# Kernel tuning notes

Measured on AMD Instinct MI355X. Metric: run time of the kernel, lower is better.

## Reference

```python
import jax, jax.numpy as jnp
import numpy as np

H, W = 16, 16
DIM = 512
HEADS = 8
DIM_HEAD = 64
INNER = HEADS * DIM_HEAD  # 512
B = 8
N = H * W  # 256
SCALE = DIM_HEAD ** -0.5
EPS = 1e-5


def _index_map(h, w):
    # index_map[n, m] = dx * (2w-1) + dy with dx = x-i+h-1, dy = y-j+w-1
    xs = np.arange(h)
    ys = np.arange(w)
    dx = xs[:, None] - xs[None, :] + h - 1            # (h, h)
    dy = ys[:, None] - ys[None, :] + w - 1            # (w, w)
    idx = dx[:, None, :, None] * (2 * w - 1) + dy[None, :, None, :]  # (h, w, h, w)
    return idx.reshape(h * w, h * w).astype(np.int32)


def setup_inputs() -> dict:
    key = jax.random.key(0)
    ks = jax.random.split(key, 5)
    x = jax.random.normal(ks[0], (B, N, DIM), dtype=jnp.float32)
    ln_g = jnp.ones((DIM,), jnp.float32)
    ln_b = jnp.zeros((DIM,), jnp.float32)
    w_qkv = jax.random.normal(ks[1], (DIM, 3 * INNER), jnp.float32) * 0.02
    unique_params = jax.random.normal(ks[2], ((2 * H - 1) * (2 * W - 1), INNER), jnp.float32) * 0.02
    w_out = jax.random.normal(ks[3], (INNER, DIM), jnp.float32) * 0.02
    b_out = jnp.zeros((DIM,), jnp.float32)
    idx_map = jnp.asarray(_index_map(H, W))  # (N, N) int32
    return {"x": x, "ln_g": ln_g, "ln_b": ln_b, "w_qkv": w_qkv,
            "unique_params": unique_params, "w_out": w_out, "b_out": b_out,
            "idx_map": idx_map}


def reference(x, ln_g, ln_b, w_qkv, unique_params, w_out, b_out, idx_map):
    b, n, _ = x.shape
    # LayerNorm
    mu = jnp.mean(x, axis=-1, keepdims=True)
    var = jnp.mean(jnp.square(x - mu), axis=-1, keepdims=True)
    xn = (x - mu) * jax.lax.rsqrt(var + EPS) * ln_g + ln_b
    # qkv projection (no bias)
    qkv = xn @ w_qkv                                  # (b, n, 3*inner)
    q, k, v = jnp.split(qkv, 3, axis=-1)
    q = q.reshape(b, n, HEADS, DIM_HEAD)
    k = k.reshape(b, n, HEADS, DIM_HEAD)
    v = v.reshape(b, n, HEADS, DIM_HEAD)
    # attention scores
    dots = jnp.einsum('bnhd,bmhd->bhnm', q, k) * SCALE
    attn = jax.nn.softmax(dots, axis=-1)              # (b, h, n, m)
    # relative-position table: (n, m, h, d)
    rpos = unique_params[idx_map].reshape(n, n, HEADS, DIM_HEAD)
    # out[b,h,n,d] = sum_m attn[b,h,n,m] * (v[b,m,h,d] + rpos[n,m,h,d])
    out = jnp.einsum('bhnm,bmhd->bnhd', attn, v) \
        + jnp.einsum('bhnm,nmhd->bnhd', attn, rpos)
    out = out.reshape(b, n, INNER)
    return out @ w_out + b_out
```

## Files before the change

### kernel.cpp

```cpp
#include <hip/hip_runtime.h>
#include <math.h>

#define NB 8
#define SEQ 256
#define DIMC 512
#define NHEAD 8
#define DHEAD 64
#define SCALEF 0.125f

typedef __attribute__((ext_vector_type(8))) short s16x8;
typedef __attribute__((ext_vector_type(4))) float f32x4;

typedef __attribute__((address_space(3))) unsigned int lds_u32_t;
typedef const __attribute__((address_space(1))) unsigned int g_u32_t;
static __device__ __forceinline__ void gl_lds16(const void* gsrc, void* ldst) {
  __builtin_amdgcn_global_load_lds((g_u32_t*)gsrc, (lds_u32_t*)ldst, 16, 0, 0);
}

static __device__ __forceinline__ unsigned short f2bf(float f) {
  union { float f; unsigned u; } c; c.f = f;
  unsigned r = c.u + 0x7FFF + ((c.u >> 16) & 1);
  return (unsigned short)(r >> 16);
}

static __device__ void tcast_body(const float* __restrict__ W,
    unsigned short* __restrict__ WT, int K, int N, int n0, int k0, int t,
    float (*tile)[65]) {
#pragma unroll
  for (int i = 0; i < 16; ++i) {
    const int idx = i * 256 + t;
    const int kl = idx >> 6, nl = idx & 63;
    tile[kl][nl] = W[(size_t)(k0 + kl) * N + n0 + nl];
  }
  __syncthreads();
#pragma unroll
  for (int i = 0; i < 16; ++i) {
    const int idx = i * 256 + t;
    const int nl = idx >> 6, kl = idx & 63;
    WT[(size_t)(n0 + nl) * K + k0 + kl] = f2bf(tile[kl][nl]);
  }
}

__global__ __launch_bounds__(256) void prep_kernel(const float* __restrict__ x,
    const float* __restrict__ g, const float* __restrict__ bta,
    const float* __restrict__ w_qkv, const float* __restrict__ w_out,
    const float* __restrict__ up, unsigned short* __restrict__ xnb,
    unsigned short* __restrict__ wqt, unsigned short* __restrict__ wot,
    unsigned short* __restrict__ upT) {
  __shared__ float tile[64][65];
  __shared__ float sh_s[4], sh_q[4];
  const int t = threadIdx.x;
  const int bid = blockIdx.x;
  if (bid < 192) {
    tcast_body(w_qkv, wqt, 512, 1536, (bid % 24) * 64, (bid / 24) * 64, t, tile);
  } else if (bid < 256) {
    const int b2 = bid - 192;
    tcast_body(w_out, wot, 512, 512, (b2 % 8) * 64, (b2 / 8) * 64, t, tile);
  } else if (bid < 384) {
    const int b2 = bid - 256;
    const int k0 = (b2 >> 3) * 64, n0 = (b2 & 7) * 64;
#pragma unroll
    for (int i = 0; i < 16; ++i) {
      const int idx = i * 256 + t;
      const int kl = idx >> 6, nl = idx & 63;
      const int k = k0 + kl;
      tile[kl][nl] = (k < 961) ? up[(size_t)k * 512 + n0 + nl] : 0.0f;
    }
    __syncthreads();
#pragma unroll
    for (int i = 0; i < 16; ++i) {
      const int idx = i * 256 + t;
      const int nl = idx >> 6, kl = idx & 63;
      if (k0 + kl < 992)
        upT[(size_t)(n0 + nl) * 992 + k0 + kl] = f2bf(tile[kl][nl]);
    }
  } else {
    const int row = bid - 384;
    const float2 v = ((const float2*)(x + (size_t)row * DIMC))[t];
    float s = v.x + v.y;
    float q = v.x * v.x + v.y * v.y;
#pragma unroll
    for (int off = 32; off > 0; off >>= 1) {
      s += __shfl_down(s, off);
      q += __shfl_down(q, off);
    }
    const int wave = t >> 6, lane = t & 63;
    if (lane == 0) { sh_s[wave] = s; sh_q[wave] = q; }
    __syncthreads();
    const float fs = sh_s[0] + sh_s[1] + sh_s[2] + sh_s[3];
    const float fq = sh_q[0] + sh_q[1] + sh_q[2] + sh_q[3];
    const float mean = fs * (1.0f / DIMC);
    const float inv = rsqrtf(fq * (1.0f / DIMC) - mean * mean + 1e-5f);
    const float2 gv = ((const float2*)g)[t];
    const float2 bv = ((const float2*)bta)[t];
    ushort2 o;
    o.x = f2bf((v.x - mean) * inv * gv.x + bv.x);
    o.y = f2bf((v.y - mean) * inv * gv.y + bv.y);
    ((ushort2*)(xnb + (size_t)row * DIMC))[t] = o;
  }
}

template <int BM, int BN, bool BIAS, bool OUTBF, bool VSPLIT>
__global__ __launch_bounds__(256) void mfma_gemm_bt(
    const unsigned short* __restrict__ A, const unsigned short* __restrict__ BT,
    const float* __restrict__ bias, void* __restrict__ Cv,
    unsigned short* __restrict__ vtb, int M, int K, int N) {
  constexpr int TR = BM / 32;
  constexpr int TC = BN / 32;
  __shared__ unsigned short As[BM * 32];
  __shared__ unsigned short Bs[BN * 32];
  const int t = threadIdx.x;
  const int wave = t >> 6, lane = t & 63;
  const int wr = wave >> 1, wc = wave & 1;
  const int bm = blockIdx.x * BM, bn = blockIdx.y * BN;

  f32x4 acc[TR][TC] = {};

  const int fr = lane & 15, q4 = lane >> 4;
  const int kBlocks = K >> 5;
  for (int kb = 0; kb < kBlocks; ++kb) {
    const int k0 = kb << 5;
    __syncthreads();
#pragma unroll
    for (int c = 0; c < (BM * 4 + 255) / 256; ++c) {
      const int p = c * 256 + t;
      if (BM * 4 % 256 == 0 || p < BM * 4) {
        const int row = p >> 2;
        const int jl = (p & 3) ^ ((row >> 1) & 3);
        gl_lds16(A + (size_t)(bm + row) * K + k0 + jl * 8,
                 As + (size_t)(c * 256 + wave * 64) * 8);
      }
    }
#pragma unroll
    for (int c = 0; c < (BN * 4 + 255) / 256; ++c) {
      const int p = c * 256 + t;
      if (BN * 4 % 256 == 0 || p < BN * 4) {
        const int row = p >> 2;
        const int jl = (p & 3) ^ ((row >> 1) & 3);
        gl_lds16(BT + (size_t)(bn + row) * K + k0 + jl * 8,
                 Bs + (size_t)(c * 256 + wave * 64) * 8);
      }
    }
    __syncthreads();
    s16x8 af[TR], bfr[TC];
#pragma unroll
    for (int i = 0; i < TR; ++i) {
      const int row = wr * (BM / 2) + i * 16 + fr;
      const int jp = q4 ^ ((row >> 1) & 3);
      af[i] = *(const s16x8*)(As + row * 32 + jp * 8);
    }
#pragma unroll
    for (int j = 0; j < TC; ++j) {
      const int row = wc * (BN / 2) + j * 16 + fr;
      const int jp = q4 ^ ((row >> 1) & 3);
      bfr[j] = *(const s16x8*)(Bs + row * 32 + jp * 8);
    }
#pragma unroll
    for (int i = 0; i < TR; ++i)
#pragma unroll
      for (int j = 0; j < TC; ++j)
        acc[i][j] = __builtin_amdgcn_mfma_f32_16x16x32_bf16(af[i], bfr[j],
                                                            acc[i][j], 0, 0, 0);
  }
  if (VSPLIT && bn >= 1024) {
#pragma unroll
    for (int i = 0; i < TR; ++i) {
#pragma unroll
      for (int j = 0; j < TC; ++j) {
        const int hc = bn - 1024 + wc * (BN / 2) + j * 16 + fr;
        const int h = hc >> 6, d = hc & 63;
#pragma unroll
        for (int r = 0; r < 4; ++r) {
          const int row = bm + wr * (BM / 2) + i * 16 + q4 * 4 + r;
          const int b = row >> 8, m = row & 255;
          vtb[(size_t)((b * 8 + h) * 64 + d) * 256 + m] = f2bf(acc[i][j][r]);
        }
      }
    }
    return;
  }
#pragma unroll
  for (int i = 0; i < TR; ++i) {
#pragma unroll
    for (int j = 0; j < TC; ++j) {
      const int col = bn + wc * (BN / 2) + j * 16 + fr;
      const float bv = BIAS ? bias[col] : 0.0f;
#pragma unroll
      for (int r = 0; r < 4; ++r) {
        const int row = bm + wr * (BM / 2) + i * 16 + q4 * 4 + r;
        if constexpr (OUTBF) {
          ((unsigned short*)Cv)[(size_t)row * N + col] = f2bf(acc[i][j][r] + bv);
        } else {
          ((float*)Cv)[(size_t)row * N + col] = acc[i][j][r] + bv;
        }
      }
    }
  }
}

#define PSTR 264
#define ASTR 552
__global__ __launch_bounds__(128) void attn_rpos_kernel(
    const unsigned short* __restrict__ qkvb,
    const unsigned short* __restrict__ vtb,
    const unsigned short* __restrict__ upT,
    unsigned short* __restrict__ ob) {
  __shared__ unsigned short ascat[32 * ASTR];
  __shared__ unsigned short p_lds[32 * PSTR];
  const int bh = blockIdx.y, b = bh >> 3, h = bh & 7;
  const int n0 = blockIdx.x * 32;
  const int t = threadIdx.x, wave = t >> 6, lane = t & 63;
  const int fr = lane & 15, q4 = lane >> 4;
  const int kwin0 = ((n0 >> 4) * 31) & ~7;

  {
    const s16x8 z = {0, 0, 0, 0, 0, 0, 0, 0};
#pragma unroll
    for (int i = 0; i < 18; ++i) {
      const int idx = i * 128 + t;
      if (idx < 32 * ASTR / 8) *(s16x8*)(ascat + idx * 8) = z;
    }
  }

  s16x8 qf[2];
  {
    const size_t qrow = (size_t)(b * SEQ + n0 + wave * 16 + fr) * 1536 + h * 64;
#pragma unroll
    for (int ks = 0; ks < 2; ++ks)
      qf[ks] = *(const s16x8*)(qkvb + qrow + ks * 32 + q4 * 8);
  }

  f32x4 s[16];
#pragma unroll
  for (int mt = 0; mt < 16; ++mt) s[mt] = (f32x4){0.f, 0.f, 0.f, 0.f};
  {
    const unsigned short* kb = qkvb + (size_t)(b * SEQ + fr) * 1536 + 512 + h * 64;
#pragma unroll
    for (int ks = 0; ks < 2; ++ks)
#pragma unroll
      for (int mt = 0; mt < 16; ++mt) {
        const s16x8 kf =
            *(const s16x8*)(kb + (size_t)mt * (16 * 1536) + ks * 32 + q4 * 8);
        s[mt] = __builtin_amdgcn_mfma_f32_16x16x32_bf16(qf[ks], kf, s[mt], 0, 0, 0);
      }
  }

  float mx[4] = {-1e30f, -1e30f, -1e30f, -1e30f};
#pragma unroll
  for (int mt = 0; mt < 16; ++mt)
#pragma unroll
    for (int r = 0; r < 4; ++r) {
      s[mt][r] *= SCALEF;
      mx[r] = fmaxf(mx[r], s[mt][r]);
    }
#pragma unroll
  for (int r = 0; r < 4; ++r) {
    mx[r] = fmaxf(mx[r], __shfl_xor(mx[r], 1));
    mx[r] = fmaxf(mx[r], __shfl_xor(mx[r], 2));
    mx[r] = fmaxf(mx[r], __shfl_xor(mx[r], 4));
    mx[r] = fmaxf(mx[r], __shfl_xor(mx[r], 8));
  }
  float sum[4] = {0.f, 0.f, 0.f, 0.f};
#pragma unroll
  for (int mt = 0; mt < 16; ++mt)
#pragma unroll
    for (int r = 0; r < 4; ++r) {
      s[mt][r] = __expf(s[mt][r] - mx[r]);
      sum[r] += s[mt][r];
    }
#pragma unroll
  for (int r = 0; r < 4; ++r) {
    sum[r] += __shfl_xor(sum[r], 1);
    sum[r] += __shfl_xor(sum[r], 2);
    sum[r] += __shfl_xor(sum[r], 4);
    sum[r] += __shfl_xor(sum[r], 8);
  }
  const float invs[4] = {1.0f / sum[0], 1.0f / sum[1], 1.0f / sum[2],
                         1.0f / sum[3]};

  __syncthreads();

  const int nb = wave * 16 + q4 * 4;
#pragma unroll
  for (int r = 0; r < 4; ++r) {
    const int n = n0 + nb + r;
    const int xn = n >> 4, yn = n & 15;
    const int cb = (xn + 15) * 31 + (yn - fr + 15) - kwin0;
    unsigned short* arow = ascat + (nb + r) * ASTR + cb;
    unsigned short* prow = p_lds + (nb + r) * PSTR + fr;
#pragma unroll
    for (int mt = 0; mt < 16; ++mt) {
      const unsigned short pb = f2bf(s[mt][r] * invs[r]);
      prow[mt * 16] = pb;
      arow[-(mt * 31)] = pb;
    }
  }
  __syncthreads();

  f32x4 o[4];
#pragma unroll
  for (int dt = 0; dt < 4; ++dt) o[dt] = (f32x4){0.f, 0.f, 0.f, 0.f};

  {
    const unsigned short* uB = upT + (size_t)(h * 64 + fr) * 992 + kwin0;
    const unsigned short* aR = ascat + (wave * 16 + fr) * ASTR;
#pragma unroll
    for (int ks = 0; ks < 17; ++ks) {
      const s16x8 af = *(const s16x8*)(aR + ks * 32 + q4 * 8);
#pragma unroll
      for (int dt = 0; dt < 4; ++dt) {
        const s16x8 bfg =
            *(const s16x8*)(uB + (size_t)dt * (16 * 992) + ks * 32 + q4 * 8);
        o[dt] = __builtin_amdgcn_mfma_f32_16x16x32_bf16(af, bfg, o[dt], 0, 0, 0);
      }
    }
  }
  {
    const unsigned short* vB = vtb + (size_t)(bh * 64 + fr) * 256;
    const unsigned short* pR = p_lds + (wave * 16 + fr) * PSTR;
#pragma unroll
    for (int ks = 0; ks < 8; ++ks) {
      const s16x8 pf = *(const s16x8*)(pR + ks * 32 + q4 * 8);
#pragma unroll
      for (int dt = 0; dt < 4; ++dt) {
        const s16x8 vfg =
            *(const s16x8*)(vB + (size_t)dt * (16 * 256) + ks * 32 + q4 * 8);
        o[dt] = __builtin_amdgcn_mfma_f32_16x16x32_bf16(pf, vfg, o[dt], 0, 0, 0);
      }
    }
  }
#pragma unroll
  for (int dt = 0; dt < 4; ++dt)
#pragma unroll
    for (int r = 0; r < 4; ++r) {
      const int n = n0 + wave * 16 + q4 * 4 + r;
      ob[(size_t)(b * SEQ + n) * DIMC + h * 64 + dt * 16 + fr] = f2bf(o[dt][r]);
    }
}

extern "C" void kernel_launch(void* const* d_in, const int* in_sizes, int n_in,
                              void* d_out, int out_size, void* d_ws,
                              size_t ws_size, hipStream_t stream) {
  const float* x = (const float*)d_in[0];
  const float* ln_g = (const float*)d_in[1];
  const float* ln_b = (const float*)d_in[2];
  const float* w_qkv = (const float*)d_in[3];
  const float* up = (const float*)d_in[4];
  const float* w_out = (const float*)d_in[5];
  const float* b_out = (const float*)d_in[6];
  float* out = (float*)d_out;

  unsigned short* u = (unsigned short*)d_ws;
  unsigned short* qkvb = u;
  unsigned short* xnb = u + 3145728;
  unsigned short* ob = u + 4194304;
  unsigned short* wqt = u + 5242880;
  unsigned short* wot = u + 6029312;
  unsigned short* upT = u + 6291456;
  unsigned short* vtb = u + 6799360;
  if (ws_size < (size_t)7847936 * sizeof(unsigned short)) return;

  prep_kernel<<<2432, 256, 0, stream>>>(x, ln_g, ln_b, w_qkv, w_out, up,
                                        xnb, wqt, wot, upT);
  mfma_gemm_bt<64, 64, false, true, true>
      <<<dim3(32, 24), 256, 0, stream>>>(xnb, wqt, nullptr, qkvb, vtb,
                                         2048, 512, 1536);
  attn_rpos_kernel<<<dim3(8, 64), 128, 0, stream>>>(qkvb, vtb, upT, ob);
  mfma_gemm_bt<64, 32, true, false, false>
      <<<dim3(32, 16), 256, 0, stream>>>(ob, wot, b_out, out, nullptr,
                                         2048, 512, 512);
}
```

Baseline: 118.3 us.

## Split attention block per query row across four waves with cross-wave softmax

The attention+relative-position kernel now handles 16 query rows per block with 4 waves instead of 32 rows with 2 waves. Each wave computes scores for a quarter of the keys, and row max and sum are combined across waves through shared memory. Each wave then produces one 16-wide slice of the head dimension, using two interleaved accumulators per product to shorten MFMA dependency chains. This doubles the grid and shrinks the rpos window to 16 k-steps, aiming for more parallelism and less redundant work, at the cost of extra barriers and reduced reuse of Q fragments.

```diff
diff --git a/kernel.cpp b/kernel.cpp
--- a/kernel.cpp
+++ b/kernel.cpp
@@ -199,59 +199,62 @@
 }
 
 #define PSTR 264
-#define ASTR 552
-__global__ __launch_bounds__(128) void attn_rpos_kernel(
+#define ASTR2 520
+__global__ __launch_bounds__(256) void attn_rpos_kernel(
     const unsigned short* __restrict__ qkvb,
     const unsigned short* __restrict__ vtb,
     const unsigned short* __restrict__ upT,
     unsigned short* __restrict__ ob) {
-  __shared__ unsigned short ascat[32 * ASTR];
-  __shared__ unsigned short p_lds[32 * PSTR];
+  __shared__ unsigned short ascat[16 * ASTR2];
+  __shared__ unsigned short p_lds[16 * PSTR];
+  __shared__ float smax[4][16], ssum[4][16];
   const int bh = blockIdx.y, b = bh >> 3, h = bh & 7;
-  const int n0 = blockIdx.x * 32;
+  const int xn = blockIdx.x;
+  const int n0 = xn * 16;
   const int t = threadIdx.x, wave = t >> 6, lane = t & 63;
   const int fr = lane & 15, q4 = lane >> 4;
-  const int kwin0 = ((n0 >> 4) * 31) & ~7;
+  const int kwin0 = (xn * 31) & ~7;
 
   {
     const s16x8 z = {0, 0, 0, 0, 0, 0, 0, 0};
 #pragma unroll
-    for (int i = 0; i < 18; ++i) {
-      const int idx = i * 128 + t;
-      if (idx < 32 * ASTR / 8) *(s16x8*)(ascat + idx * 8) = z;
+    for (int i = 0; i < 5; ++i) {
+      const int idx = i * 256 + t;
+      if (idx < 16 * ASTR2 / 8) *(s16x8*)(ascat + idx * 8) = z;
     }
   }
 
   s16x8 qf[2];
   {
-    const size_t qrow = (size_t)(b * SEQ + n0 + wave * 16 + fr) * 1536 + h * 64;
+    const size_t qrow = (size_t)(b * SEQ + n0 + fr) * 1536 + h * 64;
 #pragma unroll
     for (int ks = 0; ks < 2; ++ks)
       qf[ks] = *(const s16x8*)(qkvb + qrow + ks * 32 + q4 * 8);
   }
 
-  f32x4 s[16];
-#pragma unroll
-  for (int mt = 0; mt < 16; ++mt) s[mt] = (f32x4){0.f, 0.f, 0.f, 0.f};
-  {
-    const unsigned short* kb = qkvb + (size_t)(b * SEQ + fr) * 1536 + 512 + h * 64;
+  f32x4 s[4];
+#pragma unroll
+  for (int j = 0; j < 4; ++j) s[j] = (f32x4){0.f, 0.f, 0.f, 0.f};
+  {
+    const unsigned short* kb =
+        qkvb + (size_t)(b * SEQ + wave * 64 + fr) * 1536 + 512 + h * 64;
 #pragma unroll
     for (int ks = 0; ks < 2; ++ks)
 #pragma unroll
-      for (int mt = 0; mt < 16; ++mt) {
+      for (int j = 0; j < 4; ++j) {
         const s16x8 kf =
-            *(const s16x8*)(kb + (size_t)mt * (16 * 1536) + ks * 32 + q4 * 8);
-        s[mt] = __builtin_amdgcn_mfma_f32_16x16x32_bf16(qf[ks], kf, s[mt], 0, 0, 0);
+            *(const s16x8*)(kb + (size_t)j * (16 * 1536) + ks * 32 + q4 * 8);
+        s[j] = __builtin_amdgcn_mfma_f32_16x16x32_bf16(qf[ks], kf, s[j], 0, 0, 0);
       }
   }
 
   float mx[4] = {-1e30f, -1e30f, -1e30f, -1e30f};
 #pragma unroll
-  for (int mt = 0; mt < 16; ++mt)
+  for (int j = 0; j < 4; ++j)
 #pragma unroll
     for (int r = 0; r < 4; ++r) {
-      s[mt][r] *= SCALEF;
-      mx[r] = fmaxf(mx[r], s[mt][r]);
+      s[j][r] *= SCALEF;
+      mx[r] = fmaxf(mx[r], s[j][r]);
     }
 #pragma unroll
   for (int r = 0; r < 4; ++r) {
@@ -260,13 +263,26 @@
     mx[r] = fmaxf(mx[r], __shfl_xor(mx[r], 4));
     mx[r] = fmaxf(mx[r], __shfl_xor(mx[r], 8));
   }
+  if (fr == 0) {
+#pragma unroll
+    for (int r = 0; r < 4; ++r) smax[wave][q4 * 4 + r] = mx[r];
+  }
+  __syncthreads();
+
+  float fm[4];
+#pragma unroll
+  for (int r = 0; r < 4; ++r) {
+    const int row = q4 * 4 + r;
+    fm[r] = fmaxf(fmaxf(smax[0][row], smax[1][row]),
+                  fmaxf(smax[2][row], smax[3][row]));
+  }
   float sum[4] = {0.f, 0.f, 0.f, 0.f};
 #pragma unroll
-  for (int mt = 0; mt < 16; ++mt)
+  for (int j = 0; j < 4; ++j)
 #pragma unroll
     for (int r = 0; r < 4; ++r) {
-      s[mt][r] = __expf(s[mt][r] - mx[r]);
-      sum[r] += s[mt][r];
+      s[j][r] = __expf(s[j][r] - fm[r]);
+      sum[r] += s[j][r];
     }
 #pragma unroll
   for (int r = 0; r < 4; ++r) {
@@ -275,67 +291,73 @@
     sum[r] += __shfl_xor(sum[r], 4);
     sum[r] += __shfl_xor(sum[r], 8);
   }
-  const float invs[4] = {1.0f / sum[0], 1.0f / sum[1], 1.0f / sum[2],
-                         1.0f / sum[3]};
-
+  if (fr == 0) {
+#pragma unroll
+    for (int r = 0; r < 4; ++r) ssum[wave][q4 * 4 + r] = sum[r];
+  }
   __syncthreads();
 
-  const int nb = wave * 16 + q4 * 4;
-#pragma unroll
-  for (int r = 0; r < 4; ++r) {
-    const int n = n0 + nb + r;
-    const int xn = n >> 4, yn = n & 15;
-    const int cb = (xn + 15) * 31 + (yn - fr + 15) - kwin0;
-    unsigned short* arow = ascat + (nb + r) * ASTR + cb;
-    unsigned short* prow = p_lds + (nb + r) * PSTR + fr;
-#pragma unroll
-    for (int mt = 0; mt < 16; ++mt) {
-      const unsigned short pb = f2bf(s[mt][r] * invs[r]);
-      prow[mt * 16] = pb;
-      arow[-(mt * 31)] = pb;
+  float invs[4];
+#pragma unroll
+  for (int r = 0; r < 4; ++r) {
+    const int row = q4 * 4 + r;
+    invs[r] = 1.0f / (ssum[0][row] + ssum[1][row] + ssum[2][row] + ssum[3][row]);
+  }
+
+#pragma unroll
+  for (int j = 0; j < 4; ++j) {
+    const int mt = wave * 4 + j;
+#pragma unroll
+    for (int r = 0; r < 4; ++r) {
+      const int row = q4 * 4 + r;
+      const unsigned short pb = f2bf(s[j][r] * invs[r]);
+      p_lds[row * PSTR + mt * 16 + fr] = pb;
+      const int c = (xn - mt + 15) * 31 + (row - fr + 15) - kwin0;
+      ascat[row * ASTR2 + c] = pb;
     }
   }
   __syncthreads();
 
-  f32x4 o[4];
-#pragma unroll
-  for (int dt = 0; dt < 4; ++dt) o[dt] = (f32x4){0.f, 0.f, 0.f, 0.f};
-
-  {
-    const unsigned short* uB = upT + (size_t)(h * 64 + fr) * 992 + kwin0;
-    const unsigned short* aR = ascat + (wave * 16 + fr) * ASTR;
-#pragma unroll
-    for (int ks = 0; ks < 17; ++ks) {
+  f32x4 oA = (f32x4){0.f, 0.f, 0.f, 0.f}, oB = oA, oC = oA, oD = oA;
+  {
+    const unsigned short* uB =
+        upT + (size_t)(h * 64 + wave * 16 + fr) * 992 + kwin0;
+    const unsigned short* aR = ascat + fr * ASTR2;
+#pragma unroll
+    for (int ks = 0; ks < 8; ++ks) {
       const s16x8 af = *(const s16x8*)(aR + ks * 32 + q4 * 8);
-#pragma unroll
-      for (int dt = 0; dt < 4; ++dt) {
-        const s16x8 bfg =
-            *(const s16x8*)(uB + (size_t)dt * (16 * 992) + ks * 32 + q4 * 8);
-        o[dt] = __builtin_amdgcn_mfma_f32_16x16x32_bf16(af, bfg, o[dt], 0, 0, 0);
-      }
-    }
-  }
-  {
-    const unsigned short* vB = vtb + (size_t)(bh * 64 + fr) * 256;
-    const unsigned short* pR = p_lds + (wave * 16 + fr) * PSTR;
-#pragma unroll
-    for (int ks = 0; ks < 8; ++ks) {
+      const s16x8 bfg = *(const s16x8*)(uB + ks * 32 + q4 * 8);
+      oA = __builtin_amdgcn_mfma_f32_16x16x32_bf16(af, bfg, oA, 0, 0, 0);
+    }
+#pragma unroll
+    for (int ks = 8; ks < 16; ++ks) {
+      const s16x8 af = *(const s16x8*)(aR + ks * 32 + q4 * 8);
+      const s16x8 bfg = *(const s16x8*)(uB + ks * 32 + q4 * 8);
+      oB = __builtin_amdgcn_mfma_f32_16x16x32_bf16(af, bfg, oB, 0, 0, 0);
+    }
+  }
+  {
+    const unsigned short* vB = vtb + (size_t)(bh * 64 + wave * 16 + fr) * 256;
+    const unsigned short* pR = p_lds + fr * PSTR;
+#pragma unroll
+    for (int ks = 0; ks < 4; ++ks) {
       const s16x8 pf = *(const s16x8*)(pR + ks * 32 + q4 * 8);
-#pragma unroll
-      for (int dt = 0; dt < 4; ++dt) {
-        const s16x8 vfg =
-            *(const s16x8*)(vB + (size_t)dt * (16 * 256) + ks * 32 + q4 * 8);
-        o[dt] = __builtin_amdgcn_mfma_f32_16x16x32_bf16(pf, vfg, o[dt], 0, 0, 0);
-      }
-    }
-  }
-#pragma unroll
-  for (int dt = 0; dt < 4; ++dt)
-#pragma unroll
-    for (int r = 0; r < 4; ++r) {
-      const int n = n0 + wave * 16 + q4 * 4 + r;
-      ob[(size_t)(b * SEQ + n) * DIMC + h * 64 + dt * 16 + fr] = f2bf(o[dt][r]);
-    }
+      const s16x8 vfg = *(const s16x8*)(vB + ks * 32 + q4 * 8);
+      oC = __builtin_amdgcn_mfma_f32_16x16x32_bf16(pf, vfg, oC, 0, 0, 0);
+    }
+#pragma unroll
+    for (int ks = 4; ks < 8; ++ks) {
+      const s16x8 pf = *(const s16x8*)(pR + ks * 32 + q4 * 8);
+      const s16x8 vfg = *(const s16x8*)(vB + ks * 32 + q4 * 8);
+      oD = __builtin_amdgcn_mfma_f32_16x16x32_bf16(pf, vfg, oD, 0, 0, 0);
+    }
+  }
+  const f32x4 o = (oA + oB) + (oC + oD);
+#pragma unroll
+  for (int r = 0; r < 4; ++r) {
+    const int n = n0 + q4 * 4 + r;
+    ob[(size_t)(b * SEQ + n) * DIMC + h * 64 + wave * 16 + fr] = f2bf(o[r]);
+  }
 }
 
 extern "C" void kernel_launch(void* const* d_in, const int* in_sizes, int n_in,
@@ -365,7 +387,7 @@
   mfma_gemm_bt<64, 64, false, true, true>
       <<<dim3(32, 24), 256, 0, stream>>>(xnb, wqt, nullptr, qkvb, vtb,
                                          2048, 512, 1536);
-  attn_rpos_kernel<<<dim3(8, 64), 128, 0, stream>>>(qkvb, vtb, upT, ob);
+  attn_rpos_kernel<<<dim3(16, 64), 256, 0, stream>>>(qkvb, vtb, upT, ob);
   mfma_gemm_bt<64, 32, true, false, false>
       <<<dim3(32, 16), 256, 0, stream>>>(ob, wot, b_out, out, nullptr,
                                          2048, 512, 512);
```

Result: faster. 111.3 us (-5.9%).
